# Performance work log

Measured on AMD Instinct MI355X. Metric: run time of the kernel, lower is better.

The kernel has to match this reference:

```python
import jax, jax.numpy as jnp
import numpy as np

N = 32768      # input points
P = 16         # num_points (kernel points == max neighbors per center)
NC = 8192      # centers after fps(ratio=0.25)
E = NC * P     # edges (exactly P neighbors per center, grouped by center)
IN_F = 64
OUT_F = 128
RADIUS = 1.0
KP_EXTENT = RADIUS / 1.5


def setup_inputs() -> dict:
    key = jax.random.key(0)
    k1, k2, k3, k4, k5 = jax.random.split(key, 5)
    x = jax.random.normal(k1, (N, IN_F), dtype=jnp.float32)
    pos = jax.random.normal(k2, (N, 3), dtype=jnp.float32)
    edge_src = jax.random.randint(k3, (E,), 0, N, dtype=jnp.int32)
    # edges grouped contiguously per center, P edges each (radius() output layout)
    edge_tgt = (jnp.arange(E, dtype=jnp.int32) // P)
    # kernel point positions inside the ball of radius KP-layout scale
    kernel_pts = jax.random.uniform(k4, (P, 3), dtype=jnp.float32,
                                    minval=-0.66 * RADIUS, maxval=0.66 * RADIUS)
    # kaiming-uniform-like init for [P, in, out] per-kernel-point weights
    bound = 1.0 / np.sqrt(IN_F)
    kernel_weight = jax.random.uniform(k5, (P, IN_F, OUT_F), dtype=jnp.float32,
                                       minval=-bound, maxval=bound)
    return {"x": x, "pos": pos, "edge_src": edge_src, "edge_tgt": edge_tgt,
            "kernel_pts": kernel_pts, "kernel_weight": kernel_weight}


def reference(x, pos, edge_src, edge_tgt, kernel_pts, kernel_weight):
    n_edges = edge_src.shape[0]
    nc = n_edges // P
    # gather endpoints (message_x_and_pos: pos_i, pos_j, x_j)
    pos_i = pos[edge_tgt]                       # [E,3]
    pos_j = pos[edge_src]                       # [E,3]
    rel = (pos_i - pos_j).reshape(nc, P, 3)     # neighbors, [NC,P,3]
    # distances from every neighbor to every kernel point
    diff = rel[:, :, None, :] - kernel_pts[None, None, :, :]   # [NC,P,K,3]
    sq = jnp.sum(diff * diff, axis=-1)                          # [NC,P,K]
    # linear KP influence, clamped at 0
    all_w = jnp.maximum(1.0 - jnp.sqrt(sq) / KP_EXTENT, 0.0)
    # one-hot argmin kernel assignment (VQ-like selection)
    nn_idx = jnp.argmin(sq, axis=-1)                            # [NC,P]
    one_hot = jax.nn.one_hot(nn_idx, P, dtype=all_w.dtype)      # [NC,P,K]
    all_w = all_w * one_hot
    feat = x[edge_src].reshape(nc, P, IN_F)                     # [NC,P,in]
    # weighted_features = all_w @ feat  (contract kernel axis vs neighbor axis)
    wf = jnp.einsum('cnk,cki->cni', all_w, feat)                # [NC,P,in]
    # per-edge matmul with the argmin-selected weight matrix; one_hot selects
    # W[nn_idx] without materializing the [E,in,out] gather
    msg = jnp.einsum('cni,cnk,kio->cno', wf, one_hot, kernel_weight)  # [NC,P,out]
    # scatter-add aggregation over target centers (MessagePassing aggr='add')
    out = jax.ops.segment_sum(msg.reshape(-1, OUT_F), edge_tgt, num_segments=NC)
    return out
```

## Files before the change

### kernel.cpp

```cpp
#include <hip/hip_runtime.h>
#include <hip/hip_bf16.h>


#define P 16
#define IN_F 64
#define OUT_F 128
#define NCC 8192
#define KPE 0.6666667f

typedef short short8 __attribute__((ext_vector_type(8)));
typedef float floatx4 __attribute__((ext_vector_type(4)));

__device__ inline unsigned short f2bf(float f) {
    __hip_bfloat16 h = __float2bfloat16(f);
    return __builtin_bit_cast(unsigned short, h);
}

__global__ __launch_bounds__(256) void kconv_w(const float* __restrict__ Wf,
                                               unsigned short* __restrict__ Wb) {
    int tg = blockIdx.x * 256 + threadIdx.x;
    int m = tg >> 13;
    int n = (tg >> 6) & 127;
    int i = tg & 63;
    Wb[tg] = f2bf(Wf[(m * 64 + i) * 128 + n]);
}

__global__ __launch_bounds__(512) void kconv_main(
    const float* __restrict__ x, const float* __restrict__ pos,
    const int* __restrict__ esrc, const int* __restrict__ etgt,
    const float* __restrict__ kpts, const unsigned short* __restrict__ Wb,
    float* __restrict__ out)
{
    __shared__ float kps[48];
    __shared__ float wv[512];
    __shared__ int   nnv[512];
    __shared__ int   srcv[512];
    __shared__ float s_loc[512];
    __shared__ __align__(16) unsigned short As[32 * 72];
    __shared__ __align__(16) unsigned short Bs[128 * 72];

    const int t  = threadIdx.x;
    const int c0 = blockIdx.x * 32;

    if (t < 48) kps[t] = kpts[t];

    const int e   = c0 * P + t;
    const int src = esrc[e];
    const int tgt = etgt[e];
    float rx = __fsub_rn(pos[tgt * 3 + 0], pos[src * 3 + 0]);
    float ry = __fsub_rn(pos[tgt * 3 + 1], pos[src * 3 + 1]);
    float rz = __fsub_rn(pos[tgt * 3 + 2], pos[src * 3 + 2]);
    __syncthreads();
    float best = 1e30f; int nn = 0;
#pragma unroll
    for (int k = 0; k < 16; ++k) {
        float dx = __fsub_rn(rx, kps[k * 3 + 0]);
        float dy = __fsub_rn(ry, kps[k * 3 + 1]);
        float dz = __fsub_rn(rz, kps[k * 3 + 2]);
        float sq = __fadd_rn(__fadd_rn(__fmul_rn(dx, dx), __fmul_rn(dy, dy)),
                             __fmul_rn(dz, dz));
        if (sq < best) { best = sq; nn = k; }
    }
    float w = fmaxf(__fsub_rn(1.0f, __fdiv_rn(__fsqrt_rn(best), KPE)), 0.0f);
    wv[t] = w; nnv[t] = nn; srcv[t] = src;
    __syncthreads();

    {
        int cl = t >> 4, mm = t & 15;
        float sacc = 0.f;
#pragma unroll
        for (int n2 = 0; n2 < 16; ++n2) {
            int idx = cl * 16 + n2;
            sacc += (nnv[idx] == mm) ? wv[idx] : 0.f;
        }
        s_loc[t] = sacc;
    }
    __syncthreads();

    const float4* x4 = reinterpret_cast<const float4*>(x);
    const uint4*  wb4 = reinterpret_cast<const uint4*>(Wb);
    const int ar = t >> 4, aq = t & 15;
    const int bn = t >> 3, bsg = t & 7;
    const int bn2 = (t + 512) >> 3, bsg2 = (t + 512) & 7;

    const int wave = t >> 6, lane = t & 63;
    const int quad = lane >> 4, l16 = lane & 15;
    const int rgi = wave & 1, cgi = wave >> 1;
    const int aoff  = (rgi * 16 + l16) * 72;
    const int boff0 = (cgi * 32 + l16) * 72;
    const int boff1 = (cgi * 32 + 16 + l16) * 72;
    const int koff  = quad * 8;

    floatx4 acc0 = {0.f, 0.f, 0.f, 0.f};
    floatx4 acc1 = {0.f, 0.f, 0.f, 0.f};

    float4 xv = x4[srcv[ar * 16 + 0] * 16 + aq];
    uint4 bv0 = wb4[t];
    uint4 bv1 = wb4[t + 512];

    for (int m = 0; m < 16; ++m) {
        float sv = s_loc[ar * 16 + m];
        ushort4 av;
        av.x = f2bf(sv * xv.x); av.y = f2bf(sv * xv.y);
        av.z = f2bf(sv * xv.z); av.w = f2bf(sv * xv.w);
        *reinterpret_cast<ushort4*>(&As[ar * 72 + aq * 4]) = av;
        *reinterpret_cast<uint4*>(&Bs[bn  * 72 + bsg  * 8]) = bv0;
        *reinterpret_cast<uint4*>(&Bs[bn2 * 72 + bsg2 * 8]) = bv1;
        __syncthreads();

        if (m < 15) {
            xv  = x4[srcv[ar * 16 + m + 1] * 16 + aq];
            bv0 = wb4[(m + 1) * 1024 + t];
            bv1 = wb4[(m + 1) * 1024 + t + 512];
        }

#pragma unroll
        for (int ks = 0; ks < 2; ++ks) {
            short8 a  = *reinterpret_cast<const short8*>(&As[aoff  + ks * 32 + koff]);
            short8 b0 = *reinterpret_cast<const short8*>(&Bs[boff0 + ks * 32 + koff]);
            acc0 = __builtin_amdgcn_mfma_f32_16x16x32_bf16(a, b0, acc0, 0, 0, 0);
            short8 b1 = *reinterpret_cast<const short8*>(&Bs[boff1 + ks * 32 + koff]);
            acc1 = __builtin_amdgcn_mfma_f32_16x16x32_bf16(a, b1, acc1, 0, 0, 0);
        }
        __syncthreads();
    }

    const int colbase = cgi * 32 + l16;
    const int rowbase = c0 + rgi * 16 + quad * 4;
#pragma unroll
    for (int v = 0; v < 4; ++v) {
        out[(rowbase + v) * 128 + colbase]      = acc0[v];
        out[(rowbase + v) * 128 + colbase + 16] = acc1[v];
    }
}

extern "C" void kernel_launch(void* const* d_in, const int* in_sizes, int n_in,
                              void* d_out, int out_size, void* d_ws, size_t ws_size,
                              hipStream_t stream) {
    const float* x    = (const float*)d_in[0];
    const float* pos  = (const float*)d_in[1];
    const int*   esrc = (const int*)d_in[2];
    const int*   etgt = (const int*)d_in[3];
    const float* kpts = (const float*)d_in[4];
    const float* Wf   = (const float*)d_in[5];
    float* out = (float*)d_out;
    unsigned short* Wb = (unsigned short*)d_ws;

    hipLaunchKernelGGL(kconv_w, dim3(512), dim3(256), 0, stream, Wf, Wb);
    hipLaunchKernelGGL(kconv_main, dim3(NCC / 32), dim3(512), 0, stream,
                       x, pos, esrc, etgt, kpts, Wb, out);
}
```

Measured before the change: 82.29 us.

## Drop LDS staging in main GEMM, load fragments directly into registers

The main kernel now handles 16 centers per 256-thread block and builds MFMA A and B fragments straight from global memory into registers. This removes the LDS tile stores and the two barriers per kernel-point iteration. Per-center source indices and weights are transposed in LDS so each lane can hold all 16 in registers. The weight-conversion kernel now transposes through shared memory so its reads and writes are coalesced. In exchange, B fragments are re-read from global or cache by every block with a strided short8 pattern, and there is more register pressure.

```diff
diff --git a/kernel.cpp b/kernel.cpp
--- a/kernel.cpp
+++ b/kernel.cpp
@@ -18,29 +18,36 @@
 
 __global__ __launch_bounds__(256) void kconv_w(const float* __restrict__ Wf,
                                                unsigned short* __restrict__ Wb) {
-    int tg = blockIdx.x * 256 + threadIdx.x;
-    int m = tg >> 13;
-    int n = (tg >> 6) & 127;
-    int i = tg & 63;
-    Wb[tg] = f2bf(Wf[(m * 64 + i) * 128 + n]);
+    __shared__ float T[64][129];
+    const int m = blockIdx.x;
+    const int t = threadIdx.x;
+#pragma unroll
+    for (int it = 0; it < 32; ++it) {
+        const int idx = it * 256 + t;
+        T[idx >> 7][idx & 127] = Wf[m * 8192 + idx];
+    }
+    __syncthreads();
+#pragma unroll
+    for (int it = 0; it < 32; ++it) {
+        const int idx = it * 256 + t;
+        Wb[m * 8192 + idx] = f2bf(T[idx & 63][idx >> 6]);
+    }
 }
 
-__global__ __launch_bounds__(512) void kconv_main(
+__global__ __launch_bounds__(256, 2) void kconv_main(
     const float* __restrict__ x, const float* __restrict__ pos,
     const int* __restrict__ esrc, const int* __restrict__ etgt,
     const float* __restrict__ kpts, const unsigned short* __restrict__ Wb,
     float* __restrict__ out)
 {
     __shared__ float kps[48];
-    __shared__ float wv[512];
-    __shared__ int   nnv[512];
-    __shared__ int   srcv[512];
-    __shared__ float s_loc[512];
-    __shared__ __align__(16) unsigned short As[32 * 72];
-    __shared__ __align__(16) unsigned short Bs[128 * 72];
+    __shared__ float wv[256];
+    __shared__ int   nnv[256];
+    __shared__ float sT[256];
+    __shared__ int   srcT[256];
 
     const int t  = threadIdx.x;
-    const int c0 = blockIdx.x * 32;
+    const int c0 = blockIdx.x * 16;
 
     if (t < 48) kps[t] = kpts[t];
 
@@ -62,71 +69,71 @@
         if (sq < best) { best = sq; nn = k; }
     }
     float w = fmaxf(__fsub_rn(1.0f, __fdiv_rn(__fsqrt_rn(best), KPE)), 0.0f);
-    wv[t] = w; nnv[t] = nn; srcv[t] = src;
+    wv[t] = w; nnv[t] = nn;
+    srcT[(t & 15) * 16 + (t >> 4)] = src;
     __syncthreads();
 
     {
-        int cl = t >> 4, mm = t & 15;
+        const int cl = t >> 4, mm = t & 15;
         float sacc = 0.f;
 #pragma unroll
         for (int n2 = 0; n2 < 16; ++n2) {
-            int idx = cl * 16 + n2;
+            const int idx = cl * 16 + n2;
             sacc += (nnv[idx] == mm) ? wv[idx] : 0.f;
         }
-        s_loc[t] = sacc;
+        sT[mm * 16 + cl] = sacc;
     }
     __syncthreads();
 
-    const float4* x4 = reinterpret_cast<const float4*>(x);
-    const uint4*  wb4 = reinterpret_cast<const uint4*>(Wb);
-    const int ar = t >> 4, aq = t & 15;
-    const int bn = t >> 3, bsg = t & 7;
-    const int bn2 = (t + 512) >> 3, bsg2 = (t + 512) & 7;
+    const float4* x4  = reinterpret_cast<const float4*>(x);
+    const short8* wb8 = reinterpret_cast<const short8*>(Wb);
 
-    const int wave = t >> 6, lane = t & 63;
+    const int lane = t & 63;
+    const int cgi  = t >> 6;
     const int quad = lane >> 4, l16 = lane & 15;
-    const int rgi = wave & 1, cgi = wave >> 1;
-    const int aoff  = (rgi * 16 + l16) * 72;
-    const int boff0 = (cgi * 32 + l16) * 72;
-    const int boff1 = (cgi * 32 + 16 + l16) * 72;
-    const int koff  = quad * 8;
+
+    int   srcR[16];
+    float sR[16];
+#pragma unroll
+    for (int m = 0; m < 16; ++m) {
+        srcR[m] = srcT[m * 16 + l16];
+        sR[m]   = sT[m * 16 + l16];
+    }
 
     floatx4 acc0 = {0.f, 0.f, 0.f, 0.f};
     floatx4 acc1 = {0.f, 0.f, 0.f, 0.f};
-
-    float4 xv = x4[srcv[ar * 16 + 0] * 16 + aq];
-    uint4 bv0 = wb4[t];
-    uint4 bv1 = wb4[t + 512];
-
-    for (int m = 0; m < 16; ++m) {
-        float sv = s_loc[ar * 16 + m];
-        ushort4 av;
-        av.x = f2bf(sv * xv.x); av.y = f2bf(sv * xv.y);
-        av.z = f2bf(sv * xv.z); av.w = f2bf(sv * xv.w);
-        *reinterpret_cast<ushort4*>(&As[ar * 72 + aq * 4]) = av;
-        *reinterpret_cast<uint4*>(&Bs[bn  * 72 + bsg  * 8]) = bv0;
-        *reinterpret_cast<uint4*>(&Bs[bn2 * 72 + bsg2 * 8]) = bv1;
-        __syncthreads();
-
-        if (m < 15) {
-            xv  = x4[srcv[ar * 16 + m + 1] * 16 + aq];
-            bv0 = wb4[(m + 1) * 1024 + t];
-            bv1 = wb4[(m + 1) * 1024 + t + 512];
-        }
+    const int bc0 = cgi * 32 + l16;
+    const int bc1 = bc0 + 16;
 
 #pragma unroll
-        for (int ks = 0; ks < 2; ++ks) {
-            short8 a  = *reinterpret_cast<const short8*>(&As[aoff  + ks * 32 + koff]);
-            short8 b0 = *reinterpret_cast<const short8*>(&Bs[boff0 + ks * 32 + koff]);
-            acc0 = __builtin_amdgcn_mfma_f32_16x16x32_bf16(a, b0, acc0, 0, 0, 0);
-            short8 b1 = *reinterpret_cast<const short8*>(&Bs[boff1 + ks * 32 + koff]);
-            acc1 = __builtin_amdgcn_mfma_f32_16x16x32_bf16(a, b1, acc1, 0, 0, 0);
-        }
-        __syncthreads();
+    for (int m = 0; m < 16; ++m) {
+        const int xb = srcR[m] * 16 + quad * 2;
+        const float4 x0 = x4[xb];
+        const float4 x1 = x4[xb + 1];
+        const float4 x2 = x4[xb + 8];
+        const float4 x3 = x4[xb + 9];
+        const short8 b00 = wb8[(m * 128 + bc0) * 8 + quad];
+        const short8 b01 = wb8[(m * 128 + bc0) * 8 + quad + 4];
+        const short8 b10 = wb8[(m * 128 + bc1) * 8 + quad];
+        const short8 b11 = wb8[(m * 128 + bc1) * 8 + quad + 4];
+        const float sv = sR[m];
+        short8 a0, a1;
+        a0[0] = (short)f2bf(sv * x0.x); a0[1] = (short)f2bf(sv * x0.y);
+        a0[2] = (short)f2bf(sv * x0.z); a0[3] = (short)f2bf(sv * x0.w);
+        a0[4] = (short)f2bf(sv * x1.x); a0[5] = (short)f2bf(sv * x1.y);
+        a0[6] = (short)f2bf(sv * x1.z); a0[7] = (short)f2bf(sv * x1.w);
+        a1[0] = (short)f2bf(sv * x2.x); a1[1] = (short)f2bf(sv * x2.y);
+        a1[2] = (short)f2bf(sv * x2.z); a1[3] = (short)f2bf(sv * x2.w);
+        a1[4] = (short)f2bf(sv * x3.x); a1[5] = (short)f2bf(sv * x3.y);
+        a1[6] = (short)f2bf(sv * x3.z); a1[7] = (short)f2bf(sv * x3.w);
+        acc0 = __builtin_amdgcn_mfma_f32_16x16x32_bf16(a0, b00, acc0, 0, 0, 0);
+        acc1 = __builtin_amdgcn_mfma_f32_16x16x32_bf16(a0, b10, acc1, 0, 0, 0);
+        acc0 = __builtin_amdgcn_mfma_f32_16x16x32_bf16(a1, b01, acc0, 0, 0, 0);
+        acc1 = __builtin_amdgcn_mfma_f32_16x16x32_bf16(a1, b11, acc1, 0, 0, 0);
     }
 
     const int colbase = cgi * 32 + l16;
-    const int rowbase = c0 + rgi * 16 + quad * 4;
+    const int rowbase = c0 + quad * 4;
 #pragma unroll
     for (int v = 0; v < 4; ++v) {
         out[(rowbase + v) * 128 + colbase]      = acc0[v];
@@ -146,7 +153,7 @@
     float* out = (float*)d_out;
     unsigned short* Wb = (unsigned short*)d_ws;
 
-    hipLaunchKernelGGL(kconv_w, dim3(512), dim3(256), 0, stream, Wf, Wb);
-    hipLaunchKernelGGL(kconv_main, dim3(NCC / 32), dim3(512), 0, stream,
+    hipLaunchKernelGGL(kconv_w, dim3(16), dim3(256), 0, stream, Wf, Wb);
+    hipLaunchKernelGGL(kconv_main, dim3(NCC / 16), dim3(256), 0, stream,
                        x, pos, esrc, etgt, kpts, Wb, out);
 }
```

New measurement: 101.5 us. 23.4% more time.

## Double-buffer LDS tiles and prefetch two kernel points ahead in main loop

Applied to the files above, without the earlier changes.

Splits the A and B shared-memory tiles into two ping-pong buffers and keeps two sets of register prefetches in flight. Each iteration computes the MFMAs on one buffer while the next tile is written into the other, which halves the barriers per kernel point. The intent is to hide global-load and LDS-write latency behind matrix math. In exchange it doubles the tile LDS footprint and raises register pressure, which may reduce occupancy.

```diff
diff --git a/kernel.cpp b/kernel.cpp
--- a/kernel.cpp
+++ b/kernel.cpp
@@ -36,8 +36,8 @@
     __shared__ int   nnv[512];
     __shared__ int   srcv[512];
     __shared__ float s_loc[512];
-    __shared__ __align__(16) unsigned short As[32 * 72];
-    __shared__ __align__(16) unsigned short Bs[128 * 72];
+    __shared__ __align__(16) unsigned short As[2][32 * 72];
+    __shared__ __align__(16) unsigned short Bs[2][128 * 72];
 
     const int t  = threadIdx.x;
     const int c0 = blockIdx.x * 32;
@@ -94,34 +94,55 @@
     floatx4 acc0 = {0.f, 0.f, 0.f, 0.f};
     floatx4 acc1 = {0.f, 0.f, 0.f, 0.f};
 
-    float4 xv = x4[srcv[ar * 16 + 0] * 16 + aq];
-    uint4 bv0 = wb4[t];
-    uint4 bv1 = wb4[t + 512];
-
-    for (int m = 0; m < 16; ++m) {
-        float sv = s_loc[ar * 16 + m];
+    auto write_buf = [&](int p, int m, const float4& xv,
+                         const uint4& b0, const uint4& b1) {
+        const float sv = s_loc[ar * 16 + m];
         ushort4 av;
         av.x = f2bf(sv * xv.x); av.y = f2bf(sv * xv.y);
         av.z = f2bf(sv * xv.z); av.w = f2bf(sv * xv.w);
-        *reinterpret_cast<ushort4*>(&As[ar * 72 + aq * 4]) = av;
-        *reinterpret_cast<uint4*>(&Bs[bn  * 72 + bsg  * 8]) = bv0;
-        *reinterpret_cast<uint4*>(&Bs[bn2 * 72 + bsg2 * 8]) = bv1;
+        *reinterpret_cast<ushort4*>(&As[p][ar * 72 + aq * 4]) = av;
+        *reinterpret_cast<uint4*>(&Bs[p][bn  * 72 + bsg  * 8]) = b0;
+        *reinterpret_cast<uint4*>(&Bs[p][bn2 * 72 + bsg2 * 8]) = b1;
+    };
+    auto mfma_buf = [&](int p) {
+#pragma unroll
+        for (int ks = 0; ks < 2; ++ks) {
+            short8 a  = *reinterpret_cast<const short8*>(&As[p][aoff  + ks * 32 + koff]);
+            short8 b0 = *reinterpret_cast<const short8*>(&Bs[p][boff0 + ks * 32 + koff]);
+            acc0 = __builtin_amdgcn_mfma_f32_16x16x32_bf16(a, b0, acc0, 0, 0, 0);
+            short8 b1 = *reinterpret_cast<const short8*>(&Bs[p][boff1 + ks * 32 + koff]);
+            acc1 = __builtin_amdgcn_mfma_f32_16x16x32_bf16(a, b1, acc1, 0, 0, 0);
+        }
+    };
+
+    float4 xA  = x4[srcv[ar * 16 + 0] * 16 + aq];
+    uint4  bA0 = wb4[t];
+    uint4  bA1 = wb4[t + 512];
+    float4 xB  = x4[srcv[ar * 16 + 1] * 16 + aq];
+    uint4  bB0 = wb4[1024 + t];
+    uint4  bB1 = wb4[1024 + t + 512];
+
+    write_buf(0, 0, xA, bA0, bA1);
+    __syncthreads();
+
+#pragma unroll
+    for (int m = 0; m < 16; m += 2) {
+        if (m + 2 < 16) {
+            xA  = x4[srcv[ar * 16 + m + 2] * 16 + aq];
+            bA0 = wb4[(m + 2) * 1024 + t];
+            bA1 = wb4[(m + 2) * 1024 + t + 512];
+        }
+        mfma_buf(0);
+        write_buf(1, m + 1, xB, bB0, bB1);
         __syncthreads();
 
-        if (m < 15) {
-            xv  = x4[srcv[ar * 16 + m + 1] * 16 + aq];
-            bv0 = wb4[(m + 1) * 1024 + t];
-            bv1 = wb4[(m + 1) * 1024 + t + 512];
+        if (m + 3 < 16) {
+            xB  = x4[srcv[ar * 16 + m + 3] * 16 + aq];
+            bB0 = wb4[(m + 3) * 1024 + t];
+            bB1 = wb4[(m + 3) * 1024 + t + 512];
         }
-
-#pragma unroll
-        for (int ks = 0; ks < 2; ++ks) {
-            short8 a  = *reinterpret_cast<const short8*>(&As[aoff  + ks * 32 + koff]);
-            short8 b0 = *reinterpret_cast<const short8*>(&Bs[boff0 + ks * 32 + koff]);
-            acc0 = __builtin_amdgcn_mfma_f32_16x16x32_bf16(a, b0, acc0, 0, 0, 0);
-            short8 b1 = *reinterpret_cast<const short8*>(&Bs[boff1 + ks * 32 + koff]);
-            acc1 = __builtin_amdgcn_mfma_f32_16x16x32_bf16(a, b1, acc1, 0, 0, 0);
-        }
+        mfma_buf(1);
+        if (m + 2 < 16) write_buf(0, m + 2, xA, bA0, bA1);
         __syncthreads();
     }
 
```

After: 80.09 us. 1.03x faster.
